# Kernel optimization log

Hardware: AMD Instinct MI355X
Metric: run time of the kernel (lower is better)

Reference implementation:

```python
import jax, jax.numpy as jnp
import numpy as np

B, T, C = 4, 2048, 1024
H = 16
D = C // H  # head_dim = 64


def setup_inputs() -> dict:
    key = jax.random.key(0)
    ks = jax.random.split(key, 9)
    s = 1.0 / np.sqrt(C)
    return {
        "x": jax.random.normal(ks[0], (B, T, C), dtype=jnp.float32),
        "wq": jax.random.uniform(ks[1], (C, C), jnp.float32, -s, s),
        "bq": jax.random.uniform(ks[2], (C,), jnp.float32, -s, s),
        "wk": jax.random.uniform(ks[3], (C, C), jnp.float32, -s, s),
        "bk": jax.random.uniform(ks[4], (C,), jnp.float32, -s, s),
        "wv": jax.random.uniform(ks[5], (C, C), jnp.float32, -s, s),
        "bv": jax.random.uniform(ks[6], (C,), jnp.float32, -s, s),
        "wo": jax.random.uniform(ks[7], (C, C), jnp.float32, -s, s),
        "bo": jax.random.uniform(ks[8], (C,), jnp.float32, -s, s),
    }


def reference(x, wq, bq, wk, bk, wv, bv, wo, bo):
    # Linear layers (torch convention: y = x @ W.T + b)
    q = x @ wq.T + bq  # [B,T,C]
    k = x @ wk.T + bk
    v = x @ wv.T + bv
    # split heads -> [B,H,T,D]
    q = q.reshape(B, T, H, D).transpose(0, 2, 1, 3)
    k = k.reshape(B, T, H, D).transpose(0, 2, 1, 3)
    v = v.reshape(B, T, H, D).transpose(0, 2, 1, 3)
    scores = jnp.einsum('bhqd,bhkd->bhqk', q, k) / jnp.sqrt(jnp.float32(D))
    causal = jnp.tril(jnp.ones((T, T), dtype=bool))  # position i attends to j<=i
    scores = jnp.where(causal, scores, -jnp.inf)
    attn = jax.nn.softmax(scores, axis=-1)
    # dropout p=0.0 (eval / identity)
    out = jnp.einsum('bhqk,bhkd->bhqd', attn, v)  # [B,H,T,D]
    out = out.transpose(0, 2, 1, 3).reshape(B, T, C)
    return out @ wo.T + bo
```

## Files before the change

### kernel.cpp

```cpp
#include <hip/hip_runtime.h>
#include <stdint.h>

#define B_DIM 4
#define T_DIM 2048
#define C_DIM 1024
#define H_DIM 16
#define D_DIM 64
#define M_DIM (B_DIM * T_DIM)
#define QK_SCALE 0.18033688011112042f

typedef float f32x4 __attribute__((ext_vector_type(4)));
typedef float f32x16 __attribute__((ext_vector_type(16)));
typedef short bf16x8 __attribute__((ext_vector_type(8)));
typedef unsigned short u16;
typedef u16 u16x8 __attribute__((ext_vector_type(8)));

static __device__ __forceinline__ u16 f2b(float f) {
  uint32_t r;
  asm("v_cvt_pk_bf16_f32 %0, %1, %1" : "=v"(r) : "v"(f));
  return (u16)r;
}
static __device__ __forceinline__ uint32_t f2b2(float a, float b) {
  uint32_t r;
  asm("v_cvt_pk_bf16_f32 %0, %1, %2" : "=v"(r) : "v"(a), "v"(b));
  return r;
}
static __device__ __forceinline__ float xhalf_max(float x) {
  return fmaxf(x, __shfl_xor(x, 32, 64));
}
static __device__ __forceinline__ float xhalf_sum(float x) {
  return x + __shfl_xor(x, 32, 64);
}

static __device__ __forceinline__ void gl_lds16(const u16* g, u16* l) {
  __builtin_amdgcn_global_load_lds(
      (const __attribute__((address_space(1))) void*)g,
      (__attribute__((address_space(3))) void*)l, 16, 0, 0);
}

__global__ void k_cvt_all(const float* __restrict__ x,
                          const float* __restrict__ s0, const float* __restrict__ s1,
                          const float* __restrict__ s2, const float* __restrict__ s3,
                          u16* __restrict__ dx,
                          u16* __restrict__ d0, u16* __restrict__ d1,
                          u16* __restrict__ d2, u16* __restrict__ d3) {
  int i = blockIdx.x * blockDim.x + threadIdx.x;
  const float* s;
  u16* d;
  int j;
  if (i < (1 << 21)) {
    s = x; d = dx; j = i;
  } else {
    int k = i - (1 << 21);
    int seg = k >> 18;
    j = k & ((1 << 18) - 1);
    s = seg == 0 ? s0 : seg == 1 ? s1 : seg == 2 ? s2 : s3;
    d = seg == 0 ? d0 : seg == 1 ? d1 : seg == 2 ? d2 : d3;
  }
  float4 v = ((const float4*)s)[j];
  uint2 o;
  o.x = f2b2(v.x, v.y);
  o.y = f2b2(v.z, v.w);
  ((uint2*)d)[j] = o;
}

__global__ __launch_bounds__(256) void k_gemm_qkv(
    const u16* __restrict__ A,
    const u16* __restrict__ w0, const u16* __restrict__ w1, const u16* __restrict__ w2,
    const float* __restrict__ b0, const float* __restrict__ b1, const float* __restrict__ b2,
    u16* __restrict__ Qo, u16* __restrict__ Ko, u16* __restrict__ Vto) {
  __shared__ u16 As[128 * 32];
  __shared__ u16 Bs[128 * 32];
  const int tid = threadIdx.x;
  const int l = tid & 63;
  const int w = tid >> 6;
  const int wr = w >> 1, wc = w & 1;
  const int seg = blockIdx.x >> 3;
  const int brow = blockIdx.y * 128, bcol = (blockIdx.x & 7) * 128;
  const int lrow = l & 15, lk = l >> 4;
  const int K = C_DIM;

  const u16* Bw = seg == 0 ? w0 : seg == 1 ? w1 : w2;
  const float* bias = seg == 0 ? b0 : seg == 1 ? b1 : b2;
  const float scale = seg == 0 ? QK_SCALE : 1.f;

  f32x4 acc[4][4];
  for (int m = 0; m < 4; ++m)
    for (int n = 0; n < 4; ++n)
      acc[m][n] = (f32x4){0.f, 0.f, 0.f, 0.f};

  for (int kt = 0; kt < K; kt += 32) {
    __syncthreads();
    {
      int slot = tid;
      int r0 = slot >> 2, c0 = slot & 3;
      gl_lds16(A + (size_t)(brow + r0) * K + kt + c0 * 8, As + slot * 8);
      gl_lds16(Bw + (size_t)(bcol + r0) * K + kt + c0 * 8, Bs + slot * 8);
      int slot2 = slot + 256;
      int r1 = slot2 >> 2, c1 = slot2 & 3;
      gl_lds16(A + (size_t)(brow + r1) * K + kt + c1 * 8, As + slot2 * 8);
      gl_lds16(Bw + (size_t)(bcol + r1) * K + kt + c1 * 8, Bs + slot2 * 8);
    }
    asm volatile("s_waitcnt vmcnt(0)" ::: "memory");
    __syncthreads();

    bf16x8 af[4], bfr[4];
#pragma unroll
    for (int m = 0; m < 4; ++m)
      af[m] = *(const bf16x8*)(As + (wr * 64 + m * 16 + lrow) * 32 + lk * 8);
#pragma unroll
    for (int n = 0; n < 4; ++n)
      bfr[n] = *(const bf16x8*)(Bs + (wc * 64 + n * 16 + lrow) * 32 + lk * 8);
#pragma unroll
    for (int m = 0; m < 4; ++m) {
#pragma unroll
      for (int n = 0; n < 4; ++n)
        acc[m][n] = __builtin_amdgcn_mfma_f32_16x16x32_bf16(af[m], bfr[n], acc[m][n], 0, 0, 0);
    }
  }

#pragma unroll
  for (int m = 0; m < 4; ++m) {
    int rg0 = brow + wr * 64 + m * 16 + lk * 4;
    int bb = rg0 >> 11, tt0 = rg0 & (T_DIM - 1);
#pragma unroll
    for (int n = 0; n < 4; ++n) {
      int cg = bcol + wc * 64 + n * 16 + lrow;
      float bv = bias[cg];
      int hh = cg >> 6, dd = cg & 63;
      if (seg == 2) {
        float v0 = acc[m][n][0] + bv, v1 = acc[m][n][1] + bv;
        float v2 = acc[m][n][2] + bv, v3 = acc[m][n][3] + bv;
        uint2 pv;
        pv.x = f2b2(v0, v1);
        pv.y = f2b2(v2, v3);
        *(uint2*)(Vto + (((size_t)bb * H_DIM + hh) * D_DIM + dd) * T_DIM + tt0) = pv;
      } else {
        u16* Out = seg == 0 ? Qo : Ko;
#pragma unroll
        for (int i = 0; i < 4; ++i) {
          float val = (acc[m][n][i] + bv) * scale;
          Out[(((size_t)bb * H_DIM + hh) * T_DIM + tt0 + i) * D_DIM + dd] = f2b(val);
        }
      }
    }
  }
}

__global__ __launch_bounds__(256) void k_gemm_proj(
    const u16* __restrict__ A, const u16* __restrict__ Bw,
    const float* __restrict__ bias, float* __restrict__ Cout) {
  __shared__ u16 As[128 * 32];
  __shared__ u16 Bs[128 * 32];
  const int tid = threadIdx.x;
  const int l = tid & 63;
  const int w = tid >> 6;
  const int wr = w >> 1, wc = w & 1;
  const int brow = blockIdx.y * 128, bcol = blockIdx.x * 128;
  const int lrow = l & 15, lk = l >> 4;
  const int K = C_DIM, N = C_DIM;

  f32x4 acc[4][4];
  for (int m = 0; m < 4; ++m)
    for (int n = 0; n < 4; ++n)
      acc[m][n] = (f32x4){0.f, 0.f, 0.f, 0.f};

  for (int kt = 0; kt < K; kt += 32) {
    __syncthreads();
    {
      int slot = tid;
      int r0 = slot >> 2, c0 = slot & 3;
      gl_lds16(A + (size_t)(brow + r0) * K + kt + c0 * 8, As + slot * 8);
      gl_lds16(Bw + (size_t)(bcol + r0) * K + kt + c0 * 8, Bs + slot * 8);
      int slot2 = slot + 256;
      int r1 = slot2 >> 2, c1 = slot2 & 3;
      gl_lds16(A + (size_t)(brow + r1) * K + kt + c1 * 8, As + slot2 * 8);
      gl_lds16(Bw + (size_t)(bcol + r1) * K + kt + c1 * 8, Bs + slot2 * 8);
    }
    asm volatile("s_waitcnt vmcnt(0)" ::: "memory");
    __syncthreads();

    bf16x8 af[4], bfr[4];
#pragma unroll
    for (int m = 0; m < 4; ++m)
      af[m] = *(const bf16x8*)(As + (wr * 64 + m * 16 + lrow) * 32 + lk * 8);
#pragma unroll
    for (int n = 0; n < 4; ++n)
      bfr[n] = *(const bf16x8*)(Bs + (wc * 64 + n * 16 + lrow) * 32 + lk * 8);
#pragma unroll
    for (int m = 0; m < 4; ++m) {
#pragma unroll
      for (int n = 0; n < 4; ++n)
        acc[m][n] = __builtin_amdgcn_mfma_f32_16x16x32_bf16(af[m], bfr[n], acc[m][n], 0, 0, 0);
    }
  }

#pragma unroll
  for (int m = 0; m < 4; ++m) {
    int rg0 = brow + wr * 64 + m * 16 + lk * 4;
#pragma unroll
    for (int n = 0; n < 4; ++n) {
      int cg = bcol + wc * 64 + n * 16 + lrow;
      float bv = bias[cg];
#pragma unroll
      for (int i = 0; i < 4; ++i)
        Cout[(size_t)(rg0 + i) * N + cg] = acc[m][n][i] + bv;
    }
  }
}

__global__ __launch_bounds__(512) void k_attn(
    const u16* __restrict__ Q, const u16* __restrict__ Kg,
    const u16* __restrict__ Vt, u16* __restrict__ O) {
  __shared__ u16 Ks[2][128 * 64];
  __shared__ u16 Vs[2][64 * 128];

  const int tid = threadIdx.x;
  const int l = tid & 63;
  const int w = tid >> 6;
  const int bh = blockIdx.x;
  const int qb = 7 - blockIdx.y;
  const int q0 = qb * 256;
  const int ql = l & 31;
  const int hi = l >> 5;
  const int r0 = q0 + w * 32;
  const int qg = r0 + ql;

  const size_t qkbase = (size_t)bh * T_DIM * D_DIM;
  const size_t vtbase = (size_t)bh * D_DIM * T_DIM;

  const int sr = tid >> 3, sc = tid & 7;
  const int kcol = (sc ^ (sr & 7)) * 8;
  const int vr = tid >> 4, vc = tid & 15;
  const int vcol = (vc ^ (vr & 7)) * 8;

#define STAGE(buf, kt)                                                                    \
  {                                                                                       \
    gl_lds16(Kg + qkbase + (size_t)((kt) * 128 + sr) * D_DIM + kcol, Ks[buf] + tid * 8);  \
    gl_lds16(Kg + qkbase + (size_t)((kt) * 128 + 64 + sr) * D_DIM + kcol,                 \
             Ks[buf] + 4096 + tid * 8);                                                   \
    gl_lds16(Vt + vtbase + (size_t)vr * T_DIM + (kt) * 128 + vcol, Vs[buf] + tid * 8);    \
    gl_lds16(Vt + vtbase + (size_t)(vr + 32) * T_DIM + (kt) * 128 + vcol,                 \
             Vs[buf] + 4096 + tid * 8);                                                   \
  }

  bf16x8 qf[4];
#pragma unroll
  for (int kk = 0; kk < 4; ++kk)
    qf[kk] = *(const bf16x8*)(Q + qkbase + (size_t)qg * D_DIM + kk * 16 + hi * 8);

  f32x16 oacc[2];
#pragma unroll
  for (int dt = 0; dt < 2; ++dt)
#pragma unroll
    for (int r = 0; r < 16; ++r) oacc[dt][r] = 0.f;
  float m_run = -1e30f, l_run = 0.f;

  const int tdiag64 = r0 >> 6;
  const int nkt = (q0 >> 7) + 2;

  STAGE(0, 0);

  for (int kt = 0; kt < nkt; ++kt) {
    const int cur = kt & 1;
    if (kt + 1 < nkt) {
      STAGE(cur ^ 1, kt + 1);
      asm volatile("s_waitcnt vmcnt(4)" ::: "memory");
    } else {
      asm volatile("s_waitcnt vmcnt(0)" ::: "memory");
    }
    __syncthreads();

#pragma unroll
    for (int h2 = 0; h2 < 2; ++h2) {
      const int kt64 = kt * 2 + h2;
      if (kt64 <= tdiag64) {
        const u16* Kt = Ks[cur] + h2 * 4096;
        f32x16 s[2];
#pragma unroll
        for (int a = 0; a < 2; ++a)
#pragma unroll
          for (int r = 0; r < 16; ++r) s[a][r] = 0.f;

#pragma unroll
        for (int kk = 0; kk < 4; ++kk) {
#pragma unroll
          for (int a = 0; a < 2; ++a) {
            int row = a * 32 + ql;
            int blk = (kk * 2 + hi) ^ (row & 7);
            bf16x8 kf = *(const bf16x8*)(Kt + row * 64 + blk * 8);
            s[a] = __builtin_amdgcn_mfma_f32_32x32x16_bf16(kf, qf[kk], s[a], 0, 0, 0);
          }
        }

        if (kt64 == tdiag64) {
#pragma unroll
          for (int a = 0; a < 2; ++a) {
#pragma unroll
            for (int r = 0; r < 16; ++r) {
              int kv = kt64 * 64 + a * 32 + (r & 3) + 8 * (r >> 2) + 4 * hi;
              if (kv > qg) s[a][r] = -1e30f;
            }
          }
        }

        float t[16];
#pragma unroll
        for (int r = 0; r < 16; ++r) t[r] = fmaxf(s[0][r], s[1][r]);
#pragma unroll
        for (int r = 0; r < 8; ++r) t[r] = fmaxf(t[r], t[r + 8]);
#pragma unroll
        for (int r = 0; r < 4; ++r) t[r] = fmaxf(t[r], t[r + 4]);
        float pm = fmaxf(fmaxf(t[0], t[1]), fmaxf(t[2], t[3]));
        pm = xhalf_max(pm);

        if (__any(pm > m_run + 8.f)) {
          float mn = fmaxf(m_run, pm);
          float sc_ = exp2f(m_run - mn);
          m_run = mn;
          l_run *= sc_;
#pragma unroll
          for (int dt = 0; dt < 2; ++dt)
#pragma unroll
            for (int r = 0; r < 16; ++r) oacc[dt][r] *= sc_;
        }

        float rs0 = 0.f, rs1 = 0.f, rs2 = 0.f, rs3 = 0.f;
#pragma unroll
        for (int a = 0; a < 2; ++a) {
#pragma unroll
          for (int r = 0; r < 16; ++r) {
            float p = exp2f(s[a][r] - m_run);
            s[a][r] = p;
            if ((r & 3) == 0) rs0 += p;
            else if ((r & 3) == 1) rs1 += p;
            else if ((r & 3) == 2) rs2 += p;
            else rs3 += p;
          }
        }
        float rs = (rs0 + rs1) + (rs2 + rs3);
        l_run += xhalf_sum(rs);

#pragma unroll
        for (int kk = 0; kk < 4; ++kk) {
          const int a = kk >> 1;
          const int base = (kk & 1) * 8;
          union { uint32_t wd[4]; bf16x8 v; } pf;
#pragma unroll
          for (int i = 0; i < 2; ++i) {
            uint32_t Aw = f2b2(s[a][base + 2 * i], s[a][base + 2 * i + 1]);
            uint32_t Bw = f2b2(s[a][base + 4 + 2 * i], s[a][base + 5 + 2 * i]);
            uint32_t As_ = (uint32_t)__shfl_xor((int)Aw, 32, 64);
            uint32_t Bs_ = (uint32_t)__shfl_xor((int)Bw, 32, 64);
            pf.wd[i] = hi ? Bs_ : Aw;
            pf.wd[2 + i] = hi ? Bw : As_;
          }
#pragma unroll
          for (int dt = 0; dt < 2; ++dt) {
            int row = dt * 32 + ql;
            int chunk = (h2 * 8) + ((kk * 2 + hi) ^ (row & 7));
            bf16x8 vf = *(const bf16x8*)(Vs[cur] + row * 128 + chunk * 8);
            oacc[dt] = __builtin_amdgcn_mfma_f32_32x32x16_bf16(vf, pf.v, oacc[dt], 0, 0, 0);
          }
        }
      }
    }
    __syncthreads();
  }

  const int bb = bh >> 4, hh = bh & 15;
  const float inv = 1.f / l_run;
  u16* orow = O + ((size_t)bb * T_DIM + qg) * C_DIM + hh * D_DIM;
#pragma unroll
  for (int dt = 0; dt < 2; ++dt) {
#pragma unroll
    for (int g = 0; g < 4; ++g) {
      uint2 val;
      val.x = f2b2(oacc[dt][g * 4 + 0] * inv, oacc[dt][g * 4 + 1] * inv);
      val.y = f2b2(oacc[dt][g * 4 + 2] * inv, oacc[dt][g * 4 + 3] * inv);
      *(uint2*)(orow + dt * 32 + g * 8 + 4 * hi) = val;
    }
  }
}

extern "C" void kernel_launch(void* const* d_in, const int* in_sizes, int n_in,
                              void* d_out, int out_size, void* d_ws, size_t ws_size,
                              hipStream_t stream) {
  (void)in_sizes; (void)n_in; (void)out_size; (void)ws_size;
  const float* x  = (const float*)d_in[0];
  const float* wq = (const float*)d_in[1];
  const float* bq = (const float*)d_in[2];
  const float* wk = (const float*)d_in[3];
  const float* bk = (const float*)d_in[4];
  const float* wv = (const float*)d_in[5];
  const float* bv = (const float*)d_in[6];
  const float* wo = (const float*)d_in[7];
  const float* bo = (const float*)d_in[8];
  float* out = (float*)d_out;

  u16* xb  = (u16*)d_ws;
  u16* wqb = xb + (size_t)M_DIM * C_DIM;
  u16* wkb = wqb + (size_t)C_DIM * C_DIM;
  u16* wvb = wkb + (size_t)C_DIM * C_DIM;
  u16* wob = wvb + (size_t)C_DIM * C_DIM;
  u16* Qb  = wob + (size_t)C_DIM * C_DIM;
  u16* Kb  = Qb + (size_t)M_DIM * C_DIM;
  u16* Vtb = Kb + (size_t)M_DIM * C_DIM;
  u16* Ob  = Vtb + (size_t)M_DIM * C_DIM;

  k_cvt_all<<<12288, 256, 0, stream>>>(x, wq, wk, wv, wo, xb, wqb, wkb, wvb, wob);

  k_gemm_qkv<<<dim3(24, M_DIM / 128), 256, 0, stream>>>(
      xb, wqb, wkb, wvb, bq, bk, bv, Qb, Kb, Vtb);

  k_attn<<<dim3(B_DIM * H_DIM, 8), 512, 0, stream>>>(Qb, Kb, Vtb, Ob);
  k_gemm_proj<<<dim3(C_DIM / 128, M_DIM / 128), 256, 0, stream>>>(Ob, wob, bo, out);
}
```

Before: 198.4 us.

## Rewrite QKV and projection GEMMs with triple-buffered LDS pipeline and swizzled tiles

Both GEMM kernels move to 512-thread blocks computing 128x256 tiles with a K-step of 64, triple-buffered LDS, and global-to-LDS prefetch two steps ahead. LDS uses an XOR swizzle to avoid bank conflicts, and a block-index swizzle improves L2 reuse. MFMA sections run at raised wave priority. The aim is to hide global load latency behind compute and remove the full vmcnt(0) stall on every K step, at the cost of more LDS per block and lower occupancy.

```diff
diff --git a/kernel.cpp b/kernel.cpp
--- a/kernel.cpp
+++ b/kernel.cpp
@@ -64,68 +64,112 @@
   ((uint2*)d)[j] = o;
 }
 
-__global__ __launch_bounds__(256) void k_gemm_qkv(
+
+#define NT8 16
+
+__global__ __launch_bounds__(512) void k_gemm_qkv(
     const u16* __restrict__ A,
     const u16* __restrict__ w0, const u16* __restrict__ w1, const u16* __restrict__ w2,
     const float* __restrict__ b0, const float* __restrict__ b1, const float* __restrict__ b2,
     u16* __restrict__ Qo, u16* __restrict__ Ko, u16* __restrict__ Vto) {
-  __shared__ u16 As[128 * 32];
-  __shared__ u16 Bs[128 * 32];
+  __shared__ u16 LA[3 * 128 * 64];
+  __shared__ u16 LB[3 * 256 * 64];
   const int tid = threadIdx.x;
   const int l = tid & 63;
   const int w = tid >> 6;
-  const int wr = w >> 1, wc = w & 1;
-  const int seg = blockIdx.x >> 3;
-  const int brow = blockIdx.y * 128, bcol = (blockIdx.x & 7) * 128;
+  const int wm = w >> 2, wn = w & 3;
   const int lrow = l & 15, lk = l >> 4;
-  const int K = C_DIM;
+
+  const int bid = blockIdx.x;
+  const int swz = (bid & 7) * 96 + (bid >> 3);
+  const int row = swz & 63, col = swz >> 6;
+  const int seg = col >> 2;
+  const int brow = row * 128, bcol = (col & 3) * 256;
 
   const u16* Bw = seg == 0 ? w0 : seg == 1 ? w1 : w2;
   const float* bias = seg == 0 ? b0 : seg == 1 ? b1 : b2;
   const float scale = seg == 0 ? QK_SCALE : 1.f;
 
+  const int sr = tid >> 3, sc = tid & 7;
+  const int scg = (sc ^ (sr & 7)) * 8;
+  const int sdst = sr * 64 + sc * 8;
+
+  auto stA = [&](int buf, int h, int t) {
+    gl_lds16(A + (size_t)(brow + h * 64 + sr) * C_DIM + t * 64 + scg,
+             LA + buf * 8192 + h * 4096 + sdst);
+  };
+  auto stB = [&](int buf, int h, int t) {
+    gl_lds16(Bw + (size_t)(bcol + h * 64 + sr) * C_DIM + t * 64 + scg,
+             LB + buf * 16384 + h * 4096 + sdst);
+  };
+
   f32x4 acc[4][4];
+#pragma unroll
   for (int m = 0; m < 4; ++m)
-    for (int n = 0; n < 4; ++n)
-      acc[m][n] = (f32x4){0.f, 0.f, 0.f, 0.f};
-
-  for (int kt = 0; kt < K; kt += 32) {
-    __syncthreads();
-    {
-      int slot = tid;
-      int r0 = slot >> 2, c0 = slot & 3;
-      gl_lds16(A + (size_t)(brow + r0) * K + kt + c0 * 8, As + slot * 8);
-      gl_lds16(Bw + (size_t)(bcol + r0) * K + kt + c0 * 8, Bs + slot * 8);
-      int slot2 = slot + 256;
-      int r1 = slot2 >> 2, c1 = slot2 & 3;
-      gl_lds16(A + (size_t)(brow + r1) * K + kt + c1 * 8, As + slot2 * 8);
-      gl_lds16(Bw + (size_t)(bcol + r1) * K + kt + c1 * 8, Bs + slot2 * 8);
-    }
-    asm volatile("s_waitcnt vmcnt(0)" ::: "memory");
-    __syncthreads();
-
-    bf16x8 af[4], bfr[4];
+#pragma unroll
+    for (int n = 0; n < 4; ++n) acc[m][n] = (f32x4){0.f, 0.f, 0.f, 0.f};
+
+  stA(0, 0, 0); stA(0, 1, 0); stB(0, 0, 0); stB(0, 1, 0); stB(0, 2, 0); stB(0, 3, 0);
+  stA(1, 0, 1); stA(1, 1, 1); stB(1, 0, 1); stB(1, 1, 1); stB(1, 2, 1); stB(1, 3, 1);
+  asm volatile("s_waitcnt vmcnt(6)" ::: "memory");
+  __builtin_amdgcn_s_barrier();
+
+  int db = 0, db2 = 2;
+  for (int t = 0; t < NT8; ++t) {
+    const bool pf = (t + 2 < NT8);
+    const u16* LAb = LA + db * 8192;
+    const u16* LBb = LB + db * 16384;
+    bf16x8 af[4], bf[4];
+
+#define AF8(mm, kkk) (*(const bf16x8*)(LAb + (wm * 64 + (mm) * 16 + lrow) * 64 + \
+                                       ((((kkk) * 4 + lk) ^ (lrow & 7)) * 8)))
+#define BF8(nn, kkk) (*(const bf16x8*)(LBb + (wn * 64 + (nn) * 16 + lrow) * 64 + \
+                                       ((((kkk) * 4 + lk) ^ (lrow & 7)) * 8)))
+
+#pragma unroll
+    for (int m = 0; m < 4; ++m) af[m] = AF8(m, 0);
+#pragma unroll
+    for (int n = 0; n < 4; ++n) bf[n] = BF8(n, 0);
+    if (pf) { stA(db2, 0, t + 2); stB(db2, 0, t + 2); stB(db2, 1, t + 2); }
+    __builtin_amdgcn_s_barrier();
+    __builtin_amdgcn_s_setprio(1);
 #pragma unroll
     for (int m = 0; m < 4; ++m)
-      af[m] = *(const bf16x8*)(As + (wr * 64 + m * 16 + lrow) * 32 + lk * 8);
-#pragma unroll
-    for (int n = 0; n < 4; ++n)
-      bfr[n] = *(const bf16x8*)(Bs + (wc * 64 + n * 16 + lrow) * 32 + lk * 8);
-#pragma unroll
-    for (int m = 0; m < 4; ++m) {
 #pragma unroll
       for (int n = 0; n < 4; ++n)
-        acc[m][n] = __builtin_amdgcn_mfma_f32_16x16x32_bf16(af[m], bfr[n], acc[m][n], 0, 0, 0);
-    }
+        acc[m][n] = __builtin_amdgcn_mfma_f32_16x16x32_bf16(af[m], bf[n], acc[m][n], 0, 0, 0);
+    __builtin_amdgcn_s_setprio(0);
+    __builtin_amdgcn_s_barrier();
+
+#pragma unroll
+    for (int m = 0; m < 4; ++m) af[m] = AF8(m, 1);
+#pragma unroll
+    for (int n = 0; n < 4; ++n) bf[n] = BF8(n, 1);
+    if (pf) { stA(db2, 1, t + 2); stB(db2, 2, t + 2); stB(db2, 3, t + 2); }
+    __builtin_amdgcn_s_barrier();
+    __builtin_amdgcn_s_setprio(1);
+#pragma unroll
+    for (int m = 0; m < 4; ++m)
+#pragma unroll
+      for (int n = 0; n < 4; ++n)
+        acc[m][n] = __builtin_amdgcn_mfma_f32_16x16x32_bf16(af[m], bf[n], acc[m][n], 0, 0, 0);
+    __builtin_amdgcn_s_setprio(0);
+    if (pf) { asm volatile("s_waitcnt vmcnt(6)" ::: "memory"); }
+    else if (t + 1 < NT8) { asm volatile("s_waitcnt vmcnt(0)" ::: "memory"); }
+    __builtin_amdgcn_s_barrier();
+    db = db == 2 ? 0 : db + 1;
+    db2 = db2 == 2 ? 0 : db2 + 1;
+#undef AF8
+#undef BF8
   }
 
 #pragma unroll
   for (int m = 0; m < 4; ++m) {
-    int rg0 = brow + wr * 64 + m * 16 + lk * 4;
+    int rg0 = brow + wm * 64 + m * 16 + lk * 4;
     int bb = rg0 >> 11, tt0 = rg0 & (T_DIM - 1);
 #pragma unroll
     for (int n = 0; n < 4; ++n) {
-      int cg = bcol + wc * 64 + n * 16 + lrow;
+      int cg = bcol + wn * 64 + n * 16 + lrow;
       float bv = bias[cg];
       int hh = cg >> 6, dd = cg & 63;
       if (seg == 2) {
@@ -147,64 +191,105 @@
   }
 }
 
-__global__ __launch_bounds__(256) void k_gemm_proj(
+__global__ __launch_bounds__(512) void k_gemm_proj(
     const u16* __restrict__ A, const u16* __restrict__ Bw,
     const float* __restrict__ bias, float* __restrict__ Cout) {
-  __shared__ u16 As[128 * 32];
-  __shared__ u16 Bs[128 * 32];
+  __shared__ u16 LA[3 * 128 * 64];
+  __shared__ u16 LB[3 * 256 * 64];
   const int tid = threadIdx.x;
   const int l = tid & 63;
   const int w = tid >> 6;
-  const int wr = w >> 1, wc = w & 1;
-  const int brow = blockIdx.y * 128, bcol = blockIdx.x * 128;
+  const int wm = w >> 2, wn = w & 3;
   const int lrow = l & 15, lk = l >> 4;
-  const int K = C_DIM, N = C_DIM;
+
+  const int bid = blockIdx.x;
+  const int swz = (bid & 7) * 32 + (bid >> 3);
+  const int row = swz & 63, col = swz >> 6;
+  const int brow = row * 128, bcol = col * 256;
+
+  const int sr = tid >> 3, sc = tid & 7;
+  const int scg = (sc ^ (sr & 7)) * 8;
+  const int sdst = sr * 64 + sc * 8;
+
+  auto stA = [&](int buf, int h, int t) {
+    gl_lds16(A + (size_t)(brow + h * 64 + sr) * C_DIM + t * 64 + scg,
+             LA + buf * 8192 + h * 4096 + sdst);
+  };
+  auto stB = [&](int buf, int h, int t) {
+    gl_lds16(Bw + (size_t)(bcol + h * 64 + sr) * C_DIM + t * 64 + scg,
+             LB + buf * 16384 + h * 4096 + sdst);
+  };
 
   f32x4 acc[4][4];
+#pragma unroll
   for (int m = 0; m < 4; ++m)
-    for (int n = 0; n < 4; ++n)
-      acc[m][n] = (f32x4){0.f, 0.f, 0.f, 0.f};
-
-  for (int kt = 0; kt < K; kt += 32) {
-    __syncthreads();
-    {
-      int slot = tid;
-      int r0 = slot >> 2, c0 = slot & 3;
-      gl_lds16(A + (size_t)(brow + r0) * K + kt + c0 * 8, As + slot * 8);
-      gl_lds16(Bw + (size_t)(bcol + r0) * K + kt + c0 * 8, Bs + slot * 8);
-      int slot2 = slot + 256;
-      int r1 = slot2 >> 2, c1 = slot2 & 3;
-      gl_lds16(A + (size_t)(brow + r1) * K + kt + c1 * 8, As + slot2 * 8);
-      gl_lds16(Bw + (size_t)(bcol + r1) * K + kt + c1 * 8, Bs + slot2 * 8);
-    }
-    asm volatile("s_waitcnt vmcnt(0)" ::: "memory");
-    __syncthreads();
-
-    bf16x8 af[4], bfr[4];
+#pragma unroll
+    for (int n = 0; n < 4; ++n) acc[m][n] = (f32x4){0.f, 0.f, 0.f, 0.f};
+
+  stA(0, 0, 0); stA(0, 1, 0); stB(0, 0, 0); stB(0, 1, 0); stB(0, 2, 0); stB(0, 3, 0);
+  stA(1, 0, 1); stA(1, 1, 1); stB(1, 0, 1); stB(1, 1, 1); stB(1, 2, 1); stB(1, 3, 1);
+  asm volatile("s_waitcnt vmcnt(6)" ::: "memory");
+  __builtin_amdgcn_s_barrier();
+
+  int db = 0, db2 = 2;
+  for (int t = 0; t < NT8; ++t) {
+    const bool pf = (t + 2 < NT8);
+    const u16* LAb = LA + db * 8192;
+    const u16* LBb = LB + db * 16384;
+    bf16x8 af[4], bf[4];
+
+#define AF8(mm, kkk) (*(const bf16x8*)(LAb + (wm * 64 + (mm) * 16 + lrow) * 64 + \
+                                       ((((kkk) * 4 + lk) ^ (lrow & 7)) * 8)))
+#define BF8(nn, kkk) (*(const bf16x8*)(LBb + (wn * 64 + (nn) * 16 + lrow) * 64 + \
+                                       ((((kkk) * 4 + lk) ^ (lrow & 7)) * 8)))
+
+#pragma unroll
+    for (int m = 0; m < 4; ++m) af[m] = AF8(m, 0);
+#pragma unroll
+    for (int n = 0; n < 4; ++n) bf[n] = BF8(n, 0);
+    if (pf) { stA(db2, 0, t + 2); stB(db2, 0, t + 2); stB(db2, 1, t + 2); }
+    __builtin_amdgcn_s_barrier();
+    __builtin_amdgcn_s_setprio(1);
 #pragma unroll
     for (int m = 0; m < 4; ++m)
-      af[m] = *(const bf16x8*)(As + (wr * 64 + m * 16 + lrow) * 32 + lk * 8);
-#pragma unroll
-    for (int n = 0; n < 4; ++n)
-      bfr[n] = *(const bf16x8*)(Bs + (wc * 64 + n * 16 + lrow) * 32 + lk * 8);
-#pragma unroll
-    for (int m = 0; m < 4; ++m) {
 #pragma unroll
       for (int n = 0; n < 4; ++n)
-        acc[m][n] = __builtin_amdgcn_mfma_f32_16x16x32_bf16(af[m], bfr[n], acc[m][n], 0, 0, 0);
-    }
+        acc[m][n] = __builtin_amdgcn_mfma_f32_16x16x32_bf16(af[m], bf[n], acc[m][n], 0, 0, 0);
+    __builtin_amdgcn_s_setprio(0);
+    __builtin_amdgcn_s_barrier();
+
+#pragma unroll
+    for (int m = 0; m < 4; ++m) af[m] = AF8(m, 1);
+#pragma unroll
+    for (int n = 0; n < 4; ++n) bf[n] = BF8(n, 1);
+    if (pf) { stA(db2, 1, t + 2); stB(db2, 2, t + 2); stB(db2, 3, t + 2); }
+    __builtin_amdgcn_s_barrier();
+    __builtin_amdgcn_s_setprio(1);
+#pragma unroll
+    for (int m = 0; m < 4; ++m)
+#pragma unroll
+      for (int n = 0; n < 4; ++n)
+        acc[m][n] = __builtin_amdgcn_mfma_f32_16x16x32_bf16(af[m], bf[n], acc[m][n], 0, 0, 0);
+    __builtin_amdgcn_s_setprio(0);
+    if (pf) { asm volatile("s_waitcnt vmcnt(6)" ::: "memory"); }
+    else if (t + 1 < NT8) { asm volatile("s_waitcnt vmcnt(0)" ::: "memory"); }
+    __builtin_amdgcn_s_barrier();
+    db = db == 2 ? 0 : db + 1;
+    db2 = db2 == 2 ? 0 : db2 + 1;
+#undef AF8
+#undef BF8
   }
 
 #pragma unroll
   for (int m = 0; m < 4; ++m) {
-    int rg0 = brow + wr * 64 + m * 16 + lk * 4;
+    int rg0 = brow + wm * 64 + m * 16 + lk * 4;
 #pragma unroll
     for (int n = 0; n < 4; ++n) {
-      int cg = bcol + wc * 64 + n * 16 + lrow;
+      int cg = bcol + wn * 64 + n * 16 + lrow;
       float bv = bias[cg];
 #pragma unroll
       for (int i = 0; i < 4; ++i)
-        Cout[(size_t)(rg0 + i) * N + cg] = acc[m][n][i] + bv;
+        Cout[(size_t)(rg0 + i) * C_DIM + cg] = acc[m][n][i] + bv;
     }
   }
 }
@@ -410,9 +495,9 @@
 
   k_cvt_all<<<12288, 256, 0, stream>>>(x, wq, wk, wv, wo, xb, wqb, wkb, wvb, wob);
 
-  k_gemm_qkv<<<dim3(24, M_DIM / 128), 256, 0, stream>>>(
+  k_gemm_qkv<<<768, 512, 0, stream>>>(
       xb, wqb, wkb, wvb, bq, bk, bv, Qb, Kb, Vtb);
 
   k_attn<<<dim3(B_DIM * H_DIM, 8), 512, 0, stream>>>(Qb, Kb, Vtb, Ob);
-  k_gemm_proj<<<dim3(C_DIM / 128, M_DIM / 128), 256, 0, stream>>>(Ob, wob, bo, out);
-}
+  k_gemm_proj<<<256, 512, 0, stream>>>(Ob, wob, bo, out);
+}
```

Result: no change. 201.1 us (+1.4%).
